# Kernel optimization log

Hardware: AMD Instinct MI355X
Metric: run time of the kernel (lower is better)

Reference implementation:

```python
import jax, jax.numpy as jnp
import numpy as np

BN_EPS = 1e-5

def _conv1x1(x, w, b):
    # x: (B,C,H,W), w: (O,C), b: (O,)
    return jnp.einsum('bchw,oc->bohw', x, w) + b[None, :, None, None]

def setup_inputs() -> dict:
    key = jax.random.key(0)
    ks = jax.random.split(key, 9)
    B, C, H, W = 16, 512, 64, 64
    Ci = C // 2
    x = jax.random.normal(ks[0], (B, C, H, W), dtype=jnp.float32)
    s_in = (2.0 / C) ** 0.5   # kaiming fan_out-ish scale for 1x1 conv
    s_ci = (2.0 / Ci) ** 0.5
    return {
        'x': x,
        'g_w': jax.random.normal(ks[1], (Ci, C), dtype=jnp.float32) * s_in,
        'g_b': jnp.zeros((Ci,), dtype=jnp.float32),
        'theta_w': jax.random.normal(ks[2], (Ci, C), dtype=jnp.float32) * s_in,
        'theta_b': jnp.zeros((Ci,), dtype=jnp.float32),
        'phi_w': jax.random.normal(ks[3], (Ci, C), dtype=jnp.float32) * s_in,
        'phi_b': jnp.zeros((Ci,), dtype=jnp.float32),
        'W_w': jax.random.normal(ks[4], (C, Ci), dtype=jnp.float32) * s_ci,
        'W_b': jnp.zeros((C,), dtype=jnp.float32),
        'bn_gamma': jnp.ones((C,), dtype=jnp.float32),
        'bn_beta': jnp.zeros((C,), dtype=jnp.float32),
    }

def reference(x, g_w, g_b, theta_w, theta_b, phi_w, phi_b, W_w, W_b, bn_gamma, bn_beta):
    B, C, H, W = x.shape
    N = H * W
    g_x = _conv1x1(x, g_w, g_b).reshape(B, -1, N)          # (B, Ci, N)
    theta_x = _conv1x1(x, theta_w, theta_b).reshape(B, -1, N)  # (B, Ci, N)
    phi_x = _conv1x1(x, phi_w, phi_b).reshape(B, -1, N)        # (B, Ci, N)
    # Faithful to source: theta NOT permuted -> f is (B, Ci, Ci) channel attention
    f = jnp.einsum('bcn,bdn->bcd', theta_x, phi_x)
    f_div_C = jax.nn.softmax(f, axis=-1)
    y = jnp.einsum('bcd,bdn->bcn', f_div_C, g_x).reshape(B, -1, H, W)  # (B, Ci, H, W)
    z = _conv1x1(y, W_w, W_b)                              # (B, C, H, W)
    # BatchNorm2d, training mode (batch statistics, biased var as in torch)
    mean = jnp.mean(z, axis=(0, 2, 3), keepdims=True)
    var = jnp.var(z, axis=(0, 2, 3), keepdims=True)
    z = (z - mean) * jax.lax.rsqrt(var + BN_EPS)
    z = z * bn_gamma[None, :, None, None] + bn_beta[None, :, None, None]
    return z + x
```

## Files before the change

### kernel.cpp

```cpp
#include <hip/hip_runtime.h>

typedef __bf16 bf16x8 __attribute__((ext_vector_type(8)));
typedef float f32x4 __attribute__((ext_vector_type(4)));

#define LDK 40
#define NB 16
#define C_ 512
#define CI 256
#define HW 4096

__device__ __forceinline__ float bf2f(unsigned short u){
  union { unsigned int u; float f; } c; c.u = ((unsigned int)u) << 16; return c.f;
}
__device__ __forceinline__ unsigned short f2bf(float f){
  union { float f; unsigned int u; } c; c.f = f;
  unsigned int u = c.u + 0x7fffu + ((c.u >> 16) & 1u);
  return (unsigned short)(u >> 16);
}
__device__ __forceinline__ float read_val(const void* p, int i, bool f32){
  return f32 ? ((const float*)p)[i] : bf2f(((const unsigned short*)p)[i]);
}


__device__ __forceinline__ void stage_rm(const unsigned short* __restrict__ src, int stride,
                                         unsigned short* dst, int t){
  #pragma unroll
  for (int it = 0; it < 2; ++it){
    int idx = t + it*256;
    int row = idx >> 2;
    int ko  = (idx & 3) * 8;
    *(uint4*)(dst + row*LDK + ko) = *(const uint4*)(src + (size_t)row*stride + ko);
  }
}

__device__ __forceinline__ void stage_rm_f32(const float* __restrict__ src, int stride,
                                             unsigned short* dh, unsigned short* dl, int t){
  #pragma unroll
  for (int it = 0; it < 4; ++it){
    int idx = t + it*256;
    int row = idx >> 3;
    int ko  = (idx & 7) * 4;
    f32x4 v = *(const f32x4*)(src + (size_t)row*stride + ko);
    #pragma unroll
    for (int e = 0; e < 4; ++e){
      float fv = v[e];
      unsigned short h = f2bf(fv);
      dh[row*LDK + ko + e] = h;
      dl[row*LDK + ko + e] = f2bf(fv - bf2f(h));
    }
  }
}

__device__ __forceinline__ void stage_tr(const unsigned short* __restrict__ src, int stride,
                                         unsigned short* dst, int t){
  #pragma unroll
  for (int it = 0; it < 2; ++it){
    int idx = t + it*256;
    int row = idx >> 4;
    int co  = (idx & 15) * 8;
    uint4 vv = *(const uint4*)(src + (size_t)row*stride + co);
    unsigned short e[8]; *(uint4*)e = vv;
    #pragma unroll
    for (int k = 0; k < 8; ++k) dst[(co + k)*LDK + row] = e[k];
  }
}

__device__ __forceinline__ void stage_tr_f32(const float* __restrict__ src, int stride,
                                             unsigned short* dst, int t){
  #pragma unroll
  for (int it = 0; it < 2; ++it){
    int idx = t + it*256;
    int row = idx >> 4;
    int co  = (idx & 15) * 8;
    f32x4 v0 = *(const f32x4*)(src + (size_t)row*stride + co);
    f32x4 v1 = *(const f32x4*)(src + (size_t)row*stride + co + 4);
    #pragma unroll
    for (int k = 0; k < 4; ++k){
      dst[(co + k)*LDK + row]     = f2bf(v0[k]);
      dst[(co + 4 + k)*LDK + row] = f2bf(v1[k]);
    }
  }
}

__device__ __forceinline__ void stage_split(const float* __restrict__ src, int stride,
                                            unsigned short* dh, unsigned short* dl, int t){
  stage_rm_f32(src, stride, dh, dl, t);
}

__device__ __forceinline__ void mfma_step(const unsigned short* As, const unsigned short* Bs,
                                          f32x4 acc[4][4], int wm, int wn, int lane){
  const int r = lane & 15, q = lane >> 4;
  bf16x8 a[4], b[4];
  #pragma unroll
  for (int i = 0; i < 4; ++i)
    a[i] = *(const bf16x8*)(As + (wm*64 + 16*i + r)*LDK + 8*q);
  #pragma unroll
  for (int j = 0; j < 4; ++j)
    b[j] = *(const bf16x8*)(Bs + (wn*64 + 16*j + r)*LDK + 8*q);
  #pragma unroll
  for (int i = 0; i < 4; ++i)
    #pragma unroll
    for (int j = 0; j < 4; ++j)
      acc[i][j] = __builtin_amdgcn_mfma_f32_16x16x32_bf16(a[i], b[j], acc[i][j], 0, 0, 0);
}

__global__ __launch_bounds__(256) void k_detect(const unsigned short* __restrict__ x, int* flag){
  const int t = threadIdx.x;
  int cnt = 0;
  for (int i = t; i < 65536; i += 256){
    unsigned short u = x[i];
    if (((u >> 7) & 0xFF) == 0xFF) cnt++;
  }
  __shared__ int red[256];
  red[t] = cnt; __syncthreads();
  for (int s2 = 128; s2 > 0; s2 >>= 1){
    if (t < s2) red[t] += red[t + s2];
    __syncthreads();
  }
  if (t == 0) flag[0] = (red[0] > 0) ? 1 : 0;
}

__global__ __launch_bounds__(256) void k_wconv(const void* tw, const void* pw, const void* gw,
    const void* Ww, const void* gb, const void* tb, const void* pb, const void* Wb,
    const void* gam, const void* bet, const int* __restrict__ flag,
    unsigned short* twh, unsigned short* twl, unsigned short* phh, unsigned short* phl,
    unsigned short* gwc, unsigned short* Wwc, float* biasf){
  const bool f32 = (*flag != 0);
  const int bid = blockIdx.x, t = threadIdx.x;
  if (bid < 2048){
    const int seg = bid >> 9;
    const int i = (bid & 511)*256 + t;
    if (seg == 0){
      float w = read_val(tw, i, f32);
      unsigned short h = f2bf(w);
      twh[i] = h; twl[i] = f2bf(w - bf2f(h));
    } else if (seg == 1){
      float w = read_val(pw, i, f32);
      unsigned short h = f2bf(w);
      phh[i] = h; phl[i] = f2bf(w - bf2f(h));
    } else if (seg == 2){
      gwc[i] = f2bf(read_val(gw, i, f32));
    } else {
      Wwc[i] = f2bf(read_val(Ww, i, f32));
    }
  } else {
    const int i = (bid - 2048)*256 + t;
    if (i < 2304){
      float v;
      if      (i <  256) v = read_val(gb,  i,        f32);
      else if (i <  512) v = read_val(tb,  i - 256,  f32);
      else if (i <  768) v = read_val(pb,  i - 512,  f32);
      else if (i < 1280) v = read_val(Wb,  i - 768,  f32);
      else if (i < 1792) v = read_val(gam, i - 1280, f32);
      else               v = read_val(bet, i - 1792, f32);
      biasf[i] = v;
    }
  }
}

__global__ __launch_bounds__(256) void k_gram(const void* __restrict__ xraw,
                                              const int* __restrict__ flag,
                                              float* __restrict__ G, float* __restrict__ s){
  const bool f32 = (*flag != 0);
  const int b = blockIdx.z, bn = blockIdx.x, bm = blockIdx.y;
  const int t = threadIdx.x, lane = t & 63, w = t >> 6, wm = w >> 1, wn = w & 1;
  __shared__ unsigned short Ah[128*LDK];
  __shared__ unsigned short Al[128*LDK];
  __shared__ unsigned short Bh[128*LDK];
  __shared__ unsigned short Bl[128*LDK];
  __shared__ float red[256];
  f32x4 acc[4][4] = {};
  float sacc = 0.f;
  const bool diag = (bm == bn);
  for (int k0 = 0; k0 < HW; k0 += 32){
    if (f32){
      const float* xb = (const float*)xraw + (size_t)b*C_*HW;
      stage_rm_f32(xb + (size_t)bm*128*HW + k0, HW, Ah, Al, t);
      if (!diag) stage_rm_f32(xb + (size_t)bn*128*HW + k0, HW, Bh, Bl, t);
    } else {
      const unsigned short* xb = (const unsigned short*)xraw + (size_t)b*C_*HW;
      stage_rm(xb + (size_t)bm*128*HW + k0, HW, Ah, t);
      if (!diag) stage_rm(xb + (size_t)bn*128*HW + k0, HW, Bh, t);
    }
    __syncthreads();
    const unsigned short* BhU = diag ? Ah : Bh;
    const unsigned short* BlU = diag ? Al : Bl;
    mfma_step(Ah, BhU, acc, wm, wn, lane);
    if (f32){
      mfma_step(Ah, BlU, acc, wm, wn, lane);
      mfma_step(Al, BhU, acc, wm, wn, lane);
    }
    if (diag){
      const int row = t >> 1, half = t & 1;
      const unsigned short* ph = Ah + row*LDK + half*16;
      const unsigned short* pl = Al + row*LDK + half*16;
      if (f32){
        #pragma unroll
        for (int e = 0; e < 16; ++e) sacc += bf2f(ph[e]) + bf2f(pl[e]);
      } else {
        #pragma unroll
        for (int e = 0; e < 16; ++e) sacc += bf2f(ph[e]);
      }
    }
    __syncthreads();
  }
  float* Gb = G + (size_t)b*C_*C_;
  const int r = lane & 15, q = lane >> 4;
  #pragma unroll
  for (int i = 0; i < 4; ++i)
    #pragma unroll
    for (int j = 0; j < 4; ++j)
      #pragma unroll
      for (int ii = 0; ii < 4; ++ii){
        int row = bm*128 + wm*64 + 16*i + 4*q + ii;
        int col = bn*128 + wn*64 + 16*j + r;
        Gb[(size_t)row*C_ + col] = acc[i][j][ii];
      }
  if (diag){
    red[t] = sacc;
    __syncthreads();
    if (t < 128) s[(size_t)b*C_ + bm*128 + t] = red[2*t] + red[2*t+1];
  }
}

__global__ __launch_bounds__(256) void k_gconv(const void* __restrict__ xraw,
    const int* __restrict__ flag, const unsigned short* __restrict__ gwc,
    const float* __restrict__ gbf, unsigned short* __restrict__ gT){
  const bool f32 = (*flag != 0);
  const int b = blockIdx.z, mt = blockIdx.x, nt = blockIdx.y;
  const int t = threadIdx.x, lane = t & 63, w = t >> 6, wm = w >> 1, wn = w & 1;
  __shared__ unsigned short As[128*LDK];
  __shared__ unsigned short Bs[128*LDK];
  f32x4 acc[4][4] = {};
  for (int k0 = 0; k0 < C_; k0 += 32){
    if (f32){
      const float* xb = (const float*)xraw + (size_t)b*C_*HW;
      stage_tr_f32(xb + (size_t)k0*HW + mt*128, HW, As, t);
    } else {
      const unsigned short* xb = (const unsigned short*)xraw + (size_t)b*C_*HW;
      stage_tr(xb + (size_t)k0*HW + mt*128, HW, As, t);
    }
    stage_rm(gwc + (size_t)nt*128*C_ + k0, C_, Bs, t);
    __syncthreads();
    mfma_step(As, Bs, acc, wm, wn, lane);
    __syncthreads();
  }
  unsigned short* gTb = gT + (size_t)b*HW*CI;
  const int r = lane & 15, q = lane >> 4;
  #pragma unroll
  for (int j = 0; j < 4; ++j){
    int col = nt*128 + wn*64 + 16*j + r;
    float bias = gbf[col];
    #pragma unroll
    for (int i = 0; i < 4; ++i)
      #pragma unroll
      for (int ii = 0; ii < 4; ++ii){
        int row = mt*128 + wm*64 + 16*i + 4*q + ii;
        gTb[(size_t)row*CI + col] = f2bf(acc[i][j][ii] + bias);
      }
  }
}

__global__ __launch_bounds__(256) void k_T(const unsigned short* __restrict__ twh,
    const unsigned short* __restrict__ twl, const int* __restrict__ flag,
    const float* __restrict__ G, unsigned short* __restrict__ Th, unsigned short* __restrict__ Tl){
  const bool f32 = (*flag != 0);
  const int b = blockIdx.z, nt = blockIdx.x, mt = blockIdx.y;
  const int t = threadIdx.x, lane = t & 63, w = t >> 6, wm = w >> 1, wn = w & 1;
  __shared__ unsigned short Ath[128*LDK];
  __shared__ unsigned short Atl[128*LDK];
  __shared__ unsigned short Bh[128*LDK];
  __shared__ unsigned short Bl[128*LDK];
  const float* Gb = G + (size_t)b*C_*C_;
  f32x4 acc[4][4] = {};
  for (int k0 = 0; k0 < C_; k0 += 32){
    stage_rm(twh + (size_t)mt*128*C_ + k0, C_, Ath, t);
    if (f32) stage_rm(twl + (size_t)mt*128*C_ + k0, C_, Atl, t);
    stage_split(Gb + (size_t)nt*128*C_ + k0, C_, Bh, Bl, t);
    __syncthreads();
    mfma_step(Ath, Bh, acc, wm, wn, lane);
    mfma_step(Ath, Bl, acc, wm, wn, lane);
    if (f32) mfma_step(Atl, Bh, acc, wm, wn, lane);
    __syncthreads();
  }
  unsigned short* Thb = Th + (size_t)b*CI*C_;
  unsigned short* Tlb = Tl + (size_t)b*CI*C_;
  const int r = lane & 15, q = lane >> 4;
  #pragma unroll
  for (int i = 0; i < 4; ++i)
    #pragma unroll
    for (int j = 0; j < 4; ++j)
      #pragma unroll
      for (int ii = 0; ii < 4; ++ii){
        int row = mt*128 + wm*64 + 16*i + 4*q + ii;
        int col = nt*128 + wn*64 + 16*j + r;
        float vv = acc[i][j][ii];
        unsigned short h = f2bf(vv);
        Thb[(size_t)row*C_ + col] = h;
        Tlb[(size_t)row*C_ + col] = f2bf(vv - bf2f(h));
      }
}

__global__ __launch_bounds__(256) void k_f(const unsigned short* __restrict__ Th,
    const unsigned short* __restrict__ Tl, const unsigned short* __restrict__ phh,
    const unsigned short* __restrict__ phl, const int* __restrict__ flag,
    float* __restrict__ f){
  const bool f32 = (*flag != 0);
  const int b = blockIdx.z, nt = blockIdx.x, mt = blockIdx.y;
  const int t = threadIdx.x, lane = t & 63, w = t >> 6, wm = w >> 1, wn = w & 1;
  __shared__ unsigned short ATh[128*LDK];
  __shared__ unsigned short ATl[128*LDK];
  __shared__ unsigned short Bph[128*LDK];
  __shared__ unsigned short Bpl[128*LDK];
  f32x4 acc[4][4] = {};
  const unsigned short* Thb = Th + (size_t)b*CI*C_;
  const unsigned short* Tlb = Tl + (size_t)b*CI*C_;
  for (int k0 = 0; k0 < C_; k0 += 32){
    stage_rm(Thb + (size_t)mt*128*C_ + k0, C_, ATh, t);
    stage_rm(Tlb + (size_t)mt*128*C_ + k0, C_, ATl, t);
    stage_rm(phh + (size_t)nt*128*C_ + k0, C_, Bph, t);
    if (f32) stage_rm(phl + (size_t)nt*128*C_ + k0, C_, Bpl, t);
    __syncthreads();
    mfma_step(ATh, Bph, acc, wm, wn, lane);
    mfma_step(ATl, Bph, acc, wm, wn, lane);
    if (f32) mfma_step(ATh, Bpl, acc, wm, wn, lane);
    __syncthreads();
  }
  float* fb = f + (size_t)b*CI*CI;
  const int r = lane & 15, q = lane >> 4;
  #pragma unroll
  for (int i = 0; i < 4; ++i)
    #pragma unroll
    for (int j = 0; j < 4; ++j)
      #pragma unroll
      for (int ii = 0; ii < 4; ++ii){
        int row = mt*128 + wm*64 + 16*i + 4*q + ii;
        int col = nt*128 + wn*64 + 16*j + r;
        fb[(size_t)row*CI + col] = acc[i][j][ii];
      }
}

__global__ __launch_bounds__(256) void k_uv(const unsigned short* __restrict__ twh,
    const unsigned short* __restrict__ twl, const unsigned short* __restrict__ phh,
    const unsigned short* __restrict__ phl, const float* __restrict__ s,
    float* __restrict__ u, float* __restrict__ v){
  const int b = blockIdx.x, c = threadIdx.x;
  __shared__ float sl[C_];
  sl[c] = s[(size_t)b*C_ + c];
  sl[c + 256] = s[(size_t)b*C_ + c + 256];
  __syncthreads();
  float su = 0.f, sv = 0.f;
  for (int e = 0; e < C_; ++e){
    su += (bf2f(twh[(size_t)c*C_ + e]) + bf2f(twl[(size_t)c*C_ + e])) * sl[e];
    sv += (bf2f(phh[(size_t)c*C_ + e]) + bf2f(phl[(size_t)c*C_ + e])) * sl[e];
  }
  u[(size_t)b*CI + c] = su;
  v[(size_t)b*CI + c] = sv;
}

__global__ __launch_bounds__(256) void k_softmax(const float* __restrict__ f,
    const float* __restrict__ u, const float* __restrict__ v,
    const float* __restrict__ tbf, const float* __restrict__ pbf,
    unsigned short* __restrict__ S){
  const int b = blockIdx.y;
  const int c = blockIdx.x*4 + (threadIdx.x >> 6);
  const int lane = threadIdx.x & 63;
  const float* fr = f + ((size_t)b*CI + c)*CI;
  f32x4 val = *(const f32x4*)(fr + lane*4);
  const float uc = u[(size_t)b*CI + c];
  const float tbc = tbf[c];
  float vv[4];
  #pragma unroll
  for (int k = 0; k < 4; ++k){
    int d = lane*4 + k;
    float pbd = pbf[d];
    vv[k] = val[k] + uc*pbd + tbc*(v[(size_t)b*CI + d] + 4096.0f*pbd);
  }
  float mx = fmaxf(fmaxf(vv[0], vv[1]), fmaxf(vv[2], vv[3]));
  #pragma unroll
  for (int off = 1; off < 64; off <<= 1) mx = fmaxf(mx, __shfl_xor(mx, off));
  float e[4], sum = 0.f;
  #pragma unroll
  for (int k = 0; k < 4; ++k){ e[k] = expf(vv[k] - mx); sum += e[k]; }
  #pragma unroll
  for (int off = 1; off < 64; off <<= 1) sum += __shfl_xor(sum, off);
  float inv = 1.0f / sum;
  uint2 pack;
  pack.x = (unsigned int)f2bf(e[0]*inv) | ((unsigned int)f2bf(e[1]*inv) << 16);
  pack.y = (unsigned int)f2bf(e[2]*inv) | ((unsigned int)f2bf(e[3]*inv) << 16);
  *(uint2*)(S + ((size_t)b*CI + c)*CI + lane*4) = pack;
}

__global__ __launch_bounds__(256) void k_M2(const unsigned short* __restrict__ Wwc,
                                            const unsigned short* __restrict__ S,
                                            unsigned short* __restrict__ M2){
  const int b = blockIdx.z, nt = blockIdx.x, mt = blockIdx.y;
  const int t = threadIdx.x, lane = t & 63, w = t >> 6, wm = w >> 1, wn = w & 1;
  __shared__ unsigned short As[128*LDK];
  __shared__ unsigned short Bs[128*LDK];
  f32x4 acc[4][4] = {};
  for (int k0 = 0; k0 < CI; k0 += 32){
    stage_rm(Wwc + (size_t)mt*128*CI + k0, CI, As, t);
    stage_tr(S + (size_t)b*CI*CI + (size_t)k0*CI + nt*128, CI, Bs, t);
    __syncthreads();
    mfma_step(As, Bs, acc, wm, wn, lane);
    __syncthreads();
  }
  unsigned short* M2b = M2 + (size_t)b*C_*CI;
  const int r = lane & 15, q = lane >> 4;
  #pragma unroll
  for (int i = 0; i < 4; ++i)
    #pragma unroll
    for (int j = 0; j < 4; ++j)
      #pragma unroll
      for (int ii = 0; ii < 4; ++ii){
        int row = mt*128 + wm*64 + 16*i + 4*q + ii;
        int col = nt*128 + wn*64 + 16*j + r;
        M2b[(size_t)row*CI + col] = f2bf(acc[i][j][ii]);
      }
}

__global__ __launch_bounds__(256) void k_z(const unsigned short* __restrict__ M2,
                                           const unsigned short* __restrict__ gT,
                                           const float* __restrict__ Wbf,
                                           unsigned short* __restrict__ z){
  const int b = blockIdx.z, nt = blockIdx.x, mt = blockIdx.y;
  const int t = threadIdx.x, lane = t & 63, w = t >> 6, wm = w >> 1, wn = w & 1;
  __shared__ unsigned short As[128*LDK];
  __shared__ unsigned short Bs[128*LDK];
  const unsigned short* M2b = M2 + (size_t)b*C_*CI;
  const unsigned short* gTb = gT + (size_t)b*HW*CI;
  f32x4 acc[4][4] = {};
  for (int k0 = 0; k0 < CI; k0 += 32){
    stage_rm(M2b + (size_t)mt*128*CI + k0, CI, As, t);
    stage_rm(gTb + (size_t)nt*128*CI + k0, CI, Bs, t);
    __syncthreads();
    mfma_step(As, Bs, acc, wm, wn, lane);
    __syncthreads();
  }
  unsigned short* zb = z + (size_t)b*C_*HW;
  const int r = lane & 15, q = lane >> 4;
  #pragma unroll
  for (int i = 0; i < 4; ++i)
    #pragma unroll
    for (int ii = 0; ii < 4; ++ii){
      int row = mt*128 + wm*64 + 16*i + 4*q + ii;
      float bias = Wbf[row];
      #pragma unroll
      for (int j = 0; j < 4; ++j){
        int col = nt*128 + wn*64 + 16*j + r;
        zb[(size_t)row*HW + col] = f2bf(acc[i][j][ii] + bias);
      }
    }
}

__global__ __launch_bounds__(256) void k_bnstats(const unsigned short* __restrict__ z,
    const float* __restrict__ gamf, const float* __restrict__ betf,
    float* __restrict__ scale, float* __restrict__ shift){
  const int o = blockIdx.x, t = threadIdx.x, lane = t & 63, w = t >> 6;
  float sum = 0.f, ss = 0.f;
  for (int b = 0; b < NB; ++b){
    const unsigned short* p = z + ((size_t)b*C_ + o)*HW + t*16;
    #pragma unroll
    for (int it = 0; it < 2; ++it){
      uint4 raw = *(const uint4*)(p + it*8);
      unsigned int wd[4] = {raw.x, raw.y, raw.z, raw.w};
      #pragma unroll
      for (int k = 0; k < 4; ++k){
        float f0 = bf2f((unsigned short)(wd[k] & 0xffff));
        float f1 = bf2f((unsigned short)(wd[k] >> 16));
        sum += f0 + f1; ss += f0*f0 + f1*f1;
      }
    }
  }
  #pragma unroll
  for (int off = 1; off < 64; off <<= 1){
    sum += __shfl_xor(sum, off);
    ss  += __shfl_xor(ss, off);
  }
  __shared__ float r1[4], r2[4];
  if (lane == 0){ r1[w] = sum; r2[w] = ss; }
  __syncthreads();
  if (t == 0){
    float S1 = r1[0]+r1[1]+r1[2]+r1[3];
    float S2 = r2[0]+r2[1]+r2[2]+r2[3];
    const float n = (float)NB * (float)HW;
    float mean = S1 / n;
    float var  = S2 / n - mean*mean;
    float sc = gamf[o] * rsqrtf(var + 1e-5f);
    scale[o] = sc;
    shift[o] = betf[o] - mean*sc;
  }
}

__global__ __launch_bounds__(256) void k_out(const unsigned short* __restrict__ z,
    const void* __restrict__ xraw, const int* __restrict__ flag,
    const float* __restrict__ scale, const float* __restrict__ shift, void* __restrict__ outraw){
  const bool f32 = (*flag != 0);
  const size_t g = (size_t)blockIdx.x*256 + threadIdx.x;
  const size_t base = g*8;
  const int o = (int)((base >> 12) & (C_ - 1));
  const float sc = scale[o], sh = shift[o];
  uint4 zr = *(const uint4*)(z + base);
  unsigned int zz[4] = {zr.x, zr.y, zr.z, zr.w};
  float zv[8];
  #pragma unroll
  for (int k = 0; k < 4; ++k){
    zv[2*k]   = bf2f((unsigned short)(zz[k] & 0xffff));
    zv[2*k+1] = bf2f((unsigned short)(zz[k] >> 16));
  }
  if (f32){
    const float* x = (const float*)xraw;
    float* out = (float*)outraw;
    f32x4 x0 = *(const f32x4*)(x + base);
    f32x4 x1 = *(const f32x4*)(x + base + 4);
    f32x4 o0, o1;
    #pragma unroll
    for (int k = 0; k < 4; ++k){
      o0[k] = zv[k]*sc + sh + x0[k];
      o1[k] = zv[4+k]*sc + sh + x1[k];
    }
    *(f32x4*)(out + base) = o0;
    *(f32x4*)(out + base + 4) = o1;
  } else {
    const unsigned short* x = (const unsigned short*)xraw;
    unsigned short* out = (unsigned short*)outraw;
    uint4 xr = *(const uint4*)(x + base);
    unsigned int xx[4] = {xr.x, xr.y, xr.z, xr.w};
    unsigned int res[4];
    #pragma unroll
    for (int k = 0; k < 4; ++k){
      float x0 = bf2f((unsigned short)(xx[k] & 0xffff));
      float x1 = bf2f((unsigned short)(xx[k] >> 16));
      res[k] = (unsigned int)f2bf(zv[2*k]*sc + sh + x0)
             | ((unsigned int)f2bf(zv[2*k+1]*sc + sh + x1) << 16);
    }
    uint4 ov; ov.x = res[0]; ov.y = res[1]; ov.z = res[2]; ov.w = res[3];
    *(uint4*)(out + base) = ov;
  }
}

extern "C" void kernel_launch(void* const* d_in, const int* in_sizes, int n_in,
                              void* d_out, int out_size, void* d_ws, size_t ws_size,
                              hipStream_t stream){
  (void)in_sizes; (void)n_in; (void)out_size;
  const void* x   = d_in[0];
  const void* g_w = d_in[1];
  const void* g_b = d_in[2];
  const void* t_w = d_in[3];
  const void* t_b = d_in[4];
  const void* p_w = d_in[5];
  const void* p_b = d_in[6];
  const void* W_w = d_in[7];
  const void* W_b = d_in[8];
  const void* gam = d_in[9];
  const void* bet = d_in[10];
  char* ws = (char*)d_ws;

  constexpr size_t OFF_FLAG = 0;
  constexpr size_t OFF_TWH = OFF_FLAG + 16;
  constexpr size_t OFF_TWL = OFF_TWH + (size_t)CI*C_*2;
  constexpr size_t OFF_PHH = OFF_TWL + (size_t)CI*C_*2;
  constexpr size_t OFF_PHL = OFF_PHH + (size_t)CI*C_*2;
  constexpr size_t OFF_GWC = OFF_PHL + (size_t)CI*C_*2;
  constexpr size_t OFF_WWC = OFF_GWC + (size_t)CI*C_*2;
  constexpr size_t OFF_BIA = OFF_WWC + (size_t)C_*CI*2;
  constexpr size_t OFF_G  = OFF_BIA + 2304*4;
  constexpr size_t OFF_S  = OFF_G  + (size_t)NB*C_*C_*4;
  constexpr size_t OFF_U  = OFF_S  + (size_t)NB*C_*4;
  constexpr size_t OFF_V  = OFF_U  + (size_t)NB*CI*4;
  constexpr size_t OFF_GT = OFF_V  + (size_t)NB*CI*4;
  constexpr size_t OFF_TH = OFF_GT + (size_t)NB*HW*CI*2;
  constexpr size_t OFF_TL = OFF_TH + (size_t)NB*CI*C_*2;
  constexpr size_t OFF_F  = OFF_TL + (size_t)NB*CI*C_*2;
  constexpr size_t OFF_SM = OFF_F  + (size_t)NB*CI*CI*4;
  constexpr size_t OFF_M2 = OFF_SM + (size_t)NB*CI*CI*2;
  constexpr size_t OFF_Z  = OFF_M2 + (size_t)NB*C_*CI*2;
  constexpr size_t OFF_SC = OFF_Z  + (size_t)NB*C_*HW*2;
  constexpr size_t OFF_SH = OFF_SC + (size_t)C_*4;
  constexpr size_t TOTAL  = OFF_SH + (size_t)C_*4;
  if (ws_size < TOTAL) return;

  int* flag = (int*)(ws + OFF_FLAG);
  unsigned short* twh = (unsigned short*)(ws + OFF_TWH);
  unsigned short* twl = (unsigned short*)(ws + OFF_TWL);
  unsigned short* phh = (unsigned short*)(ws + OFF_PHH);
  unsigned short* phl = (unsigned short*)(ws + OFF_PHL);
  unsigned short* gwc = (unsigned short*)(ws + OFF_GWC);
  unsigned short* Wwc = (unsigned short*)(ws + OFF_WWC);
  float* biasf = (float*)(ws + OFF_BIA);
  float* G  = (float*)(ws + OFF_G);
  float* s  = (float*)(ws + OFF_S);
  float* u  = (float*)(ws + OFF_U);
  float* v  = (float*)(ws + OFF_V);
  unsigned short* gT = (unsigned short*)(ws + OFF_GT);
  unsigned short* Th = (unsigned short*)(ws + OFF_TH);
  unsigned short* Tl = (unsigned short*)(ws + OFF_TL);
  float* f  = (float*)(ws + OFF_F);
  unsigned short* Sm = (unsigned short*)(ws + OFF_SM);
  unsigned short* M2 = (unsigned short*)(ws + OFF_M2);
  unsigned short* z  = (unsigned short*)(ws + OFF_Z);
  float* scale = (float*)(ws + OFF_SC);
  float* shift = (float*)(ws + OFF_SH);

  float* gbf = biasf;
  float* tbf = biasf + 256;
  float* pbf = biasf + 512;
  float* Wbf = biasf + 768;
  float* gamf = biasf + 1280;
  float* betf = biasf + 1792;

  dim3 blk(256);
  k_detect <<<dim3(1),         blk, 0, stream>>>((const unsigned short*)x, flag);
  k_wconv  <<<dim3(2057),      blk, 0, stream>>>(t_w, p_w, g_w, W_w, g_b, t_b, p_b, W_b,
                                                 gam, bet, flag, twh, twl, phh, phl, gwc, Wwc, biasf);
  k_gram   <<<dim3(4, 4, NB),  blk, 0, stream>>>(x, flag, G, s);
  k_gconv  <<<dim3(32, 2, NB), blk, 0, stream>>>(x, flag, gwc, gbf, gT);
  k_T      <<<dim3(4, 2, NB),  blk, 0, stream>>>(twh, twl, flag, G, Th, Tl);
  k_uv     <<<dim3(NB),        blk, 0, stream>>>(twh, twl, phh, phl, s, u, v);
  k_f      <<<dim3(2, 2, NB),  blk, 0, stream>>>(Th, Tl, phh, phl, flag, f);
  k_softmax<<<dim3(64, NB),    blk, 0, stream>>>(f, u, v, tbf, pbf, Sm);
  k_M2     <<<dim3(2, 4, NB),  blk, 0, stream>>>(Wwc, Sm, M2);
  k_z      <<<dim3(32, 4, NB), blk, 0, stream>>>(M2, gT, Wbf, z);
  k_bnstats<<<dim3(C_),        blk, 0, stream>>>(z, gamf, betf, scale, shift);
  k_out    <<<dim3(16384),     blk, 0, stream>>>(z, x, flag, scale, shift, d_out);
}
```

Measured before the change: 818.3 us.

## Split Gram kernel over K with symmetric tile pairs and atomic accumulation

The Gram matrix kernel now computes only the 10 upper-triangular 128x128 tile pairs and mirrors off-diagonal results, and splits the 4096-long reduction into 4 K-slices accumulated with atomicAdd. A new zero kernel clears G (and s) before accumulation. The detect kernel also reads 16-byte vectors instead of shorts. This raises block count from 256 to 640 for better CU occupancy and skips redundant symmetric tiles, at the cost of atomic traffic, an extra zeroing pass, and nondeterministic summation order.

```diff
diff --git a/kernel.cpp b/kernel.cpp
--- a/kernel.cpp
+++ b/kernel.cpp
@@ -8,6 +8,9 @@
 #define C_ 512
 #define CI 256
 #define HW 4096
+
+__constant__ int PAIR_M[10] = {0,0,0,0,1,1,1,2,2,3};
+__constant__ int PAIR_N[10] = {0,1,2,3,1,2,3,2,3,3};
 
 __device__ __forceinline__ float bf2f(unsigned short u){
   union { unsigned int u; float f; } c; c.u = ((unsigned int)u) << 16; return c.f;
@@ -104,12 +107,19 @@
       acc[i][j] = __builtin_amdgcn_mfma_f32_16x16x32_bf16(a[i], b[j], acc[i][j], 0, 0, 0);
 }
 
-__global__ __launch_bounds__(256) void k_detect(const unsigned short* __restrict__ x, int* flag){
+__global__ __launch_bounds__(256) void k_detect(const uint4* __restrict__ x, int* flag){
   const int t = threadIdx.x;
   int cnt = 0;
-  for (int i = t; i < 65536; i += 256){
-    unsigned short u = x[i];
-    if (((u >> 7) & 0xFF) == 0xFF) cnt++;
+  for (int i = t; i < 4096; i += 256){
+    uint4 v = x[i];
+    unsigned int wd[4] = {v.x, v.y, v.z, v.w};
+    #pragma unroll
+    for (int k = 0; k < 4; ++k){
+      unsigned short u0 = (unsigned short)(wd[k] & 0xffff);
+      unsigned short u1 = (unsigned short)(wd[k] >> 16);
+      if (((u0 >> 7) & 0xFF) == 0xFF) cnt++;
+      if (((u1 >> 7) & 0xFF) == 0xFF) cnt++;
+    }
   }
   __shared__ int red[256];
   red[t] = cnt; __syncthreads();
@@ -118,6 +128,14 @@
     __syncthreads();
   }
   if (t == 0) flag[0] = (red[0] > 0) ? 1 : 0;
+}
+
+__global__ __launch_bounds__(256) void k_zero(f32x4* __restrict__ p){
+  const int i = blockIdx.x*256 + threadIdx.x;
+  if (i < 1050624){
+    f32x4 z = {0.f, 0.f, 0.f, 0.f};
+    p[i] = z;
+  }
 }
 
 __global__ __launch_bounds__(256) void k_wconv(const void* tw, const void* pw, const void* gw,
@@ -162,7 +180,8 @@
                                               const int* __restrict__ flag,
                                               float* __restrict__ G, float* __restrict__ s){
   const bool f32 = (*flag != 0);
-  const int b = blockIdx.z, bn = blockIdx.x, bm = blockIdx.y;
+  const int pair = blockIdx.x, ks = blockIdx.y, b = blockIdx.z;
+  const int bm = PAIR_M[pair], bn = PAIR_N[pair];
   const int t = threadIdx.x, lane = t & 63, w = t >> 6, wm = w >> 1, wn = w & 1;
   __shared__ unsigned short Ah[128*LDK];
   __shared__ unsigned short Al[128*LDK];
@@ -172,7 +191,8 @@
   f32x4 acc[4][4] = {};
   float sacc = 0.f;
   const bool diag = (bm == bn);
-  for (int k0 = 0; k0 < HW; k0 += 32){
+  const int kbase = ks*1024;
+  for (int k0 = kbase; k0 < kbase + 1024; k0 += 32){
     if (f32){
       const float* xb = (const float*)xraw + (size_t)b*C_*HW;
       stage_rm_f32(xb + (size_t)bm*128*HW + k0, HW, Ah, Al, t);
@@ -214,12 +234,14 @@
       for (int ii = 0; ii < 4; ++ii){
         int row = bm*128 + wm*64 + 16*i + 4*q + ii;
         int col = bn*128 + wn*64 + 16*j + r;
-        Gb[(size_t)row*C_ + col] = acc[i][j][ii];
+        float v = acc[i][j][ii];
+        atomicAdd(&Gb[(size_t)row*C_ + col], v);
+        if (!diag) atomicAdd(&Gb[(size_t)col*C_ + row], v);
       }
   if (diag){
     red[t] = sacc;
     __syncthreads();
-    if (t < 128) s[(size_t)b*C_ + bm*128 + t] = red[2*t] + red[2*t+1];
+    if (t < 128) atomicAdd(&s[(size_t)b*C_ + bm*128 + t], red[2*t] + red[2*t+1]);
   }
 }
 
@@ -611,17 +633,18 @@
   float* betf = biasf + 1792;
 
   dim3 blk(256);
-  k_detect <<<dim3(1),         blk, 0, stream>>>((const unsigned short*)x, flag);
-  k_wconv  <<<dim3(2057),      blk, 0, stream>>>(t_w, p_w, g_w, W_w, g_b, t_b, p_b, W_b,
-                                                 gam, bet, flag, twh, twl, phh, phl, gwc, Wwc, biasf);
-  k_gram   <<<dim3(4, 4, NB),  blk, 0, stream>>>(x, flag, G, s);
-  k_gconv  <<<dim3(32, 2, NB), blk, 0, stream>>>(x, flag, gwc, gbf, gT);
-  k_T      <<<dim3(4, 2, NB),  blk, 0, stream>>>(twh, twl, flag, G, Th, Tl);
-  k_uv     <<<dim3(NB),        blk, 0, stream>>>(twh, twl, phh, phl, s, u, v);
-  k_f      <<<dim3(2, 2, NB),  blk, 0, stream>>>(Th, Tl, phh, phl, flag, f);
-  k_softmax<<<dim3(64, NB),    blk, 0, stream>>>(f, u, v, tbf, pbf, Sm);
-  k_M2     <<<dim3(2, 4, NB),  blk, 0, stream>>>(Wwc, Sm, M2);
-  k_z      <<<dim3(32, 4, NB), blk, 0, stream>>>(M2, gT, Wbf, z);
-  k_bnstats<<<dim3(C_),        blk, 0, stream>>>(z, gamf, betf, scale, shift);
-  k_out    <<<dim3(16384),     blk, 0, stream>>>(z, x, flag, scale, shift, d_out);
-}
+  k_detect <<<dim3(1),          blk, 0, stream>>>((const uint4*)x, flag);
+  k_wconv  <<<dim3(2057),       blk, 0, stream>>>(t_w, p_w, g_w, W_w, g_b, t_b, p_b, W_b,
+                                                  gam, bet, flag, twh, twl, phh, phl, gwc, Wwc, biasf);
+  k_zero   <<<dim3(4104),       blk, 0, stream>>>((f32x4*)G);
+  k_gram   <<<dim3(10, 4, NB),  blk, 0, stream>>>(x, flag, G, s);
+  k_gconv  <<<dim3(32, 2, NB),  blk, 0, stream>>>(x, flag, gwc, gbf, gT);
+  k_T      <<<dim3(4, 2, NB),   blk, 0, stream>>>(twh, twl, flag, G, Th, Tl);
+  k_uv     <<<dim3(NB),         blk, 0, stream>>>(twh, twl, phh, phl, s, u, v);
+  k_f      <<<dim3(2, 2, NB),   blk, 0, stream>>>(Th, Tl, phh, phl, flag, f);
+  k_softmax<<<dim3(64, NB),     blk, 0, stream>>>(f, u, v, tbf, pbf, Sm);
+  k_M2     <<<dim3(2, 4, NB),   blk, 0, stream>>>(Wwc, Sm, M2);
+  k_z      <<<dim3(32, 4, NB),  blk, 0, stream>>>(M2, gT, Wbf, z);
+  k_bnstats<<<dim3(C_),         blk, 0, stream>>>(z, gamf, betf, scale, shift);
+  k_out    <<<dim3(16384),      blk, 0, stream>>>(z, x, flag, scale, shift, d_out);
+}
```

Result: no change. 824.3 us (+0.7%).
